# Optimization experiments

Measured on AMD Instinct MI355X. Metric: run time of the kernel, lower is better.

Reference implementation:

```python
import jax, jax.numpy as jnp
import numpy as np

B, S, D, H = 2, 2048, 2048, 16
DK = D // H


def setup_inputs() -> dict:
    key = jax.random.key(0)
    k1, k2, k3 = jax.random.split(key, 3)
    x = jax.random.normal(k1, (B, S, D), dtype=jnp.float32)
    # trunc-normal in the original; plain normal with matching std is fine for a numeric baseline
    std_qkv = 2.0 / (DK + D)  # note: original passes variance as std to trunc_normal_
    W_qkv = jax.random.normal(k2, (3 * D, D), dtype=jnp.float32) * std_qkv
    W_o = jax.random.normal(k3, (D, D), dtype=jnp.float32) * (1.0 / D)
    return {"x": x, "W_qkv": W_qkv, "W_o": W_o}


def reference(x, W_qkv, W_o):
    b, s, d = x.shape
    # fused QKV projection: y = x @ W_qkv^T
    qkv = jnp.einsum('bsd,ed->bse', x, W_qkv)  # [b, s, 3d]
    q, k, v = jnp.split(qkv, 3, axis=-1)
    # [b, s, d] -> [b, h, s, dk]
    def to_heads(t):
        return t.reshape(b, s, H, DK).transpose(0, 2, 1, 3)
    q, k, v = to_heads(q), to_heads(k), to_heads(v)
    scores = jnp.einsum('bhqd,bhkd->bhqk', q, k) / np.sqrt(DK).astype(np.float32)
    causal = jnp.tril(jnp.ones((s, s), dtype=bool))
    scores = jnp.where(causal, scores, -jnp.inf)
    att = jax.nn.softmax(scores, axis=-1)
    out = jnp.einsum('bhqk,bhkd->bhqd', att, v)  # [b, h, s, dk]
    out = out.transpose(0, 2, 1, 3).reshape(b, s, d)
    return jnp.einsum('bsd,od->bso', out, W_o)
```

## Files before the change

kernel.cpp:

```cpp
#include <hip/hip_runtime.h>

typedef _Float16 f16;
typedef _Float16 f16x4 __attribute__((ext_vector_type(4)));
typedef _Float16 f16x8 __attribute__((ext_vector_type(8)));
typedef float    f32x4 __attribute__((ext_vector_type(4)));

#define MFMA_F16(a,b,c) __builtin_amdgcn_mfma_f32_16x16x32_f16((a),(b),(c),0,0,0)

static constexpr int B_  = 2;
static constexpr int S_  = 2048;
static constexpr int D_  = 2048;
static constexpr int H_  = 16;
static constexpr int DK_ = 128;
static constexpr int K_  = 2048;

__device__ __forceinline__ void gload_lds16(const void* g, void* l) {
  __builtin_amdgcn_global_load_lds(
      (const __attribute__((address_space(1))) void*)g,
      (__attribute__((address_space(3))) void*)l, 16, 0, 0);
}

__global__ __launch_bounds__(256) void cast_f16_kernel(const float* __restrict__ in,
                                                       f16* __restrict__ out, int n4) {
  int i = blockIdx.x * 256 + threadIdx.x;
  int stride = gridDim.x * 256;
  for (int j = i; j < n4; j += stride) {
    float4 v = reinterpret_cast<const float4*>(in)[j];
    f16x4 o = {(f16)v.x, (f16)v.y, (f16)v.z, (f16)v.w};
    reinterpret_cast<f16x4*>(out)[j] = o;
  }
}

__device__ __forceinline__ void gemm_core(const f16* __restrict__ A, const f16* __restrict__ Bw,
                                          int brow, int bcol, f16* As, f16* Bs,
                                          f32x4 (&acc)[4][4]) {
  const int tid = threadIdx.x;
  const int w = tid >> 6, l = tid & 63;
  const int lg = l >> 4, lr = l & 15;
  const int wr = w >> 1, wc = w & 1;
#pragma unroll
  for (int mi = 0; mi < 4; ++mi)
#pragma unroll
    for (int ni = 0; ni < 4; ++ni) acc[mi][ni] = (f32x4){0.f, 0.f, 0.f, 0.f};

  const int rA = brow * 128 + (l >> 2);
  const int rB = bcol * 128 + (l >> 2);
  const int ck = (l & 3) * 8;

  for (int kt = 0; kt < K_ / 32; ++kt) {
    __syncthreads();
#pragma unroll
    for (int i = 0; i < 2; ++i) {
      const int c = w + i * 4;
      gload_lds16(A  + (size_t)(rA + c * 16) * K_ + kt * 32 + ck, As + c * 512);
      gload_lds16(Bw + (size_t)(rB + c * 16) * K_ + kt * 32 + ck, Bs + c * 512);
    }
    __syncthreads();
    f16x8 af[4], bf[4];
#pragma unroll
    for (int mi = 0; mi < 4; ++mi)
      af[mi] = *(const f16x8*)(As + (wr * 64 + mi * 16 + lr) * 32 + lg * 8);
#pragma unroll
    for (int ni = 0; ni < 4; ++ni)
      bf[ni] = *(const f16x8*)(Bs + (wc * 64 + ni * 16 + lr) * 32 + lg * 8);
#pragma unroll
    for (int mi = 0; mi < 4; ++mi)
#pragma unroll
      for (int ni = 0; ni < 4; ++ni)
        acc[mi][ni] = MFMA_F16(af[mi], bf[ni], acc[mi][ni]);
  }
}

__global__ __launch_bounds__(256) void gemm_qkv_kernel(const f16* __restrict__ xb,
                                                       const f16* __restrict__ wqkv,
                                                       f16* __restrict__ Q,
                                                       f16* __restrict__ Kk,
                                                       f16* __restrict__ V) {
  __shared__ __align__(16) f16 As[4096];
  __shared__ __align__(16) f16 Bs[4096];
  const int bid = blockIdx.x;
  const int swz = (bid & 7) * (1536 / 8) + (bid >> 3);
  const int brow = swz / 48, bcol = swz % 48;

  f32x4 acc[4][4];
  gemm_core(xb, wqkv, brow, bcol, As, Bs, acc);

  const int tid = threadIdx.x;
  const int w = tid >> 6, l = tid & 63;
  const int lg = l >> 4, lr = l & 15;
  const int wr = w >> 1, wc = w & 1;

  const int which = bcol / 16;
  const int h = bcol % 16;
  f16* outp = (which == 0) ? Q : ((which == 1) ? Kk : V);
  const float scale = (which == 0) ? 0.08838834764831845f : 1.0f;

#pragma unroll
  for (int mi = 0; mi < 4; ++mi) {
    const int mbase = brow * 128 + wr * 64 + mi * 16 + lg * 4;
#pragma unroll
    for (int ni = 0; ni < 4; ++ni) {
      const int dk = wc * 64 + ni * 16 + lr;
#pragma unroll
      for (int r = 0; r < 4; ++r) {
        const int mm = mbase + r;
        const int b = mm >> 11, s = mm & 2047;
        outp[(((size_t)b * H_ + h) * S_ + s) * DK_ + dk] = (f16)(acc[mi][ni][r] * scale);
      }
    }
  }
}

__global__ __launch_bounds__(256) void gemm_out_kernel(const f16* __restrict__ ab,
                                                       const f16* __restrict__ wo,
                                                       float* __restrict__ out) {
  __shared__ __align__(16) f16 As[4096];
  __shared__ __align__(16) f16 Bs[4096];
  const int bid = blockIdx.x;
  const int swz = (bid & 7) * (512 / 8) + (bid >> 3);
  const int brow = swz / 16, bcol = swz % 16;

  f32x4 acc[4][4];
  gemm_core(ab, wo, brow, bcol, As, Bs, acc);

  const int tid = threadIdx.x;
  const int w = tid >> 6, l = tid & 63;
  const int lg = l >> 4, lr = l & 15;
  const int wr = w >> 1, wc = w & 1;

#pragma unroll
  for (int mi = 0; mi < 4; ++mi) {
    const int mbase = brow * 128 + wr * 64 + mi * 16 + lg * 4;
#pragma unroll
    for (int ni = 0; ni < 4; ++ni) {
      const int n = bcol * 128 + wc * 64 + ni * 16 + lr;
#pragma unroll
      for (int r = 0; r < 4; ++r)
        out[(size_t)(mbase + r) * D_ + n] = acc[mi][ni][r];
    }
  }
}

__global__ __launch_bounds__(256) void transpose_v_kernel(const f16* __restrict__ V,
                                                          f16* __restrict__ Vt) {
  const int bid = blockIdx.x;
  const int dt = bid & 1;
  const int st = (bid >> 1) & 31;
  const int bh = bid >> 6;
  __shared__ __align__(16) f16 t[64][72];
  const int tid = threadIdx.x;
#pragma unroll
  for (int i = 0; i < 2; ++i) {
    const int chunk = i * 256 + tid;
    const int row = chunk >> 3, c8 = chunk & 7;
    f16x8 v = *(const f16x8*)(V + ((size_t)bh * S_ + st * 64 + row) * DK_ + dt * 64 + c8 * 8);
    *(f16x8*)&t[row][c8 * 8] = v;
  }
  __syncthreads();
#pragma unroll
  for (int i = 0; i < 2; ++i) {
    const int chunk = i * 256 + tid;
    const int row = chunk >> 3, c8 = chunk & 7;
    f16x8 v;
#pragma unroll
    for (int jj = 0; jj < 8; ++jj) v[jj] = t[c8 * 8 + jj][row];
    *(f16x8*)(Vt + ((size_t)bh * DK_ + dt * 64 + row) * S_ + st * 64 + c8 * 8) = v;
  }
}

__global__ __launch_bounds__(256) void attn_kernel(const f16* __restrict__ Q,
                                                   const f16* __restrict__ Kg,
                                                   const f16* __restrict__ Vt,
                                                   f16* __restrict__ O) {
  __shared__ __align__(16) unsigned char Ks[64 * 256];
  __shared__ __align__(16) unsigned char Vs[128 * 128];
  __shared__ __align__(16) unsigned char Ps[4][16 * 128];

  const int bid = blockIdx.x;
  const int pr = bid & 15;
  const int h  = (bid >> 4) & 15;
  const int b  = bid >> 8;
  const int bh = b * H_ + h;
  const int tid = threadIdx.x;
  const int w = tid >> 6, l = tid & 63;
  const int lg = l >> 4, lr = l & 15;

  for (int half = 0; half < 2; ++half) {
    const int qt = half ? (31 - pr) : pr;

    const f16* Qg = Q + ((size_t)bh * S_ + qt * 64 + w * 16) * DK_;
    f16x8 qf[4];
#pragma unroll
    for (int kd = 0; kd < 4; ++kd)
      qf[kd] = *(const f16x8*)(Qg + (size_t)lr * DK_ + kd * 32 + lg * 8);

    f32x4 o[8];
#pragma unroll
    for (int n = 0; n < 8; ++n) o[n] = (f32x4){0.f, 0.f, 0.f, 0.f};
    float mrun[4] = {-1e30f, -1e30f, -1e30f, -1e30f};
    float lrun[4] = {0.f, 0.f, 0.f, 0.f};

    const int ntiles = qt + 1;
    for (int kt = 0; kt < ntiles; ++kt) {
      __syncthreads();
      const f16* Kt = Kg + ((size_t)bh * S_ + kt * 64) * DK_;
#pragma unroll
      for (int i = 0; i < 4; ++i) {
        const int chunk = i * 256 + tid;
        const int row = chunk >> 4, c8 = chunk & 15;
        uint4 v = *(const uint4*)(Kt + (size_t)row * DK_ + c8 * 8);
        *(uint4*)(Ks + row * 256 + ((c8 * 16) ^ ((row & 7) << 4))) = v;
      }
      const f16* Vtt = Vt + (size_t)bh * DK_ * S_ + kt * 64;
#pragma unroll
      for (int i = 0; i < 4; ++i) {
        const int chunk = i * 256 + tid;
        const int row = chunk >> 3, c8 = chunk & 7;
        uint4 v = *(const uint4*)(Vtt + (size_t)row * S_ + c8 * 8);
        *(uint4*)(Vs + row * 128 + ((c8 * 16) ^ ((row & 7) << 4))) = v;
      }
      __syncthreads();

      f32x4 s[4];
#pragma unroll
      for (int j = 0; j < 4; ++j) s[j] = (f32x4){0.f, 0.f, 0.f, 0.f};
#pragma unroll
      for (int j = 0; j < 4; ++j) {
        const int row = j * 16 + lr;
#pragma unroll
        for (int kd = 0; kd < 4; ++kd) {
          f16x8 kf = *(const f16x8*)(Ks + row * 256 + ((kd * 64 + lg * 16) ^ ((row & 7) << 4)));
          s[j] = MFMA_F16(qf[kd], kf, s[j]);
        }
      }
      if (kt == qt) {
#pragma unroll
        for (int j = 0; j < 4; ++j) {
          const int col = j * 16 + lr;
#pragma unroll
          for (int r = 0; r < 4; ++r) {
            const int qrow = w * 16 + lg * 4 + r;
            if (col > qrow) s[j][r] = -1e30f;
          }
        }
      }
      float scl[4];
#pragma unroll
      for (int r = 0; r < 4; ++r) {
        float m0 = fmaxf(fmaxf(s[0][r], s[1][r]), fmaxf(s[2][r], s[3][r]));
#pragma unroll
        for (int msk = 1; msk < 16; msk <<= 1) m0 = fmaxf(m0, __shfl_xor(m0, msk, 64));
        const float nm = fmaxf(mrun[r], m0);
        scl[r] = __expf(mrun[r] - nm);
        mrun[r] = nm;
      }
      float rs[4] = {0.f, 0.f, 0.f, 0.f};
#pragma unroll
      for (int j = 0; j < 4; ++j) {
#pragma unroll
        for (int r = 0; r < 4; ++r) {
          const float p = __expf(fmaxf(s[j][r] - mrun[r], -80.f));
          rs[r] += p;
          const int row = lg * 4 + r;
          const int cb = (j * 16 + lr) * 2;
          *(f16*)(Ps[w] + row * 128 + (cb ^ ((row & 7) << 4))) = (f16)p;
        }
      }
#pragma unroll
      for (int r = 0; r < 4; ++r) {
        float t = rs[r];
#pragma unroll
        for (int msk = 1; msk < 16; msk <<= 1) t += __shfl_xor(t, msk, 64);
        lrun[r] = lrun[r] * scl[r] + t;
      }
#pragma unroll
      for (int n = 0; n < 8; ++n)
#pragma unroll
        for (int r = 0; r < 4; ++r) o[n][r] *= scl[r];

      asm volatile("s_waitcnt lgkmcnt(0)" ::: "memory");

#pragma unroll
      for (int ks = 0; ks < 2; ++ks) {
        f16x8 pf = *(const f16x8*)(Ps[w] + lr * 128 + ((ks * 64 + lg * 16) ^ ((lr & 7) << 4)));
#pragma unroll
        for (int n = 0; n < 8; ++n) {
          const int row = n * 16 + lr;
          f16x8 vf = *(const f16x8*)(Vs + row * 128 + ((ks * 64 + lg * 16) ^ ((row & 7) << 4)));
          o[n] = MFMA_F16(pf, vf, o[n]);
        }
      }
    }

#pragma unroll
    for (int r = 0; r < 4; ++r) {
      const float inv = 1.0f / lrun[r];
      const int srow = qt * 64 + w * 16 + lg * 4 + r;
      f16* op = O + ((size_t)b * S_ + srow) * D_ + h * DK_;
#pragma unroll
      for (int n = 0; n < 8; ++n) op[n * 16 + lr] = (f16)(o[n][r] * inv);
    }
  }
}

extern "C" void kernel_launch(void* const* d_in, const int* in_sizes, int n_in,
                              void* d_out, int out_size, void* d_ws, size_t ws_size,
                              hipStream_t stream) {
  const float* x    = (const float*)d_in[0];
  const float* wqkv = (const float*)d_in[1];
  const float* wo   = (const float*)d_in[2];
  float* out = (float*)d_out;
  char* ws = (char*)d_ws;

  f16* xb     = (f16*)(ws + 0);
  f16* wqkvb  = (f16*)(ws + 16777216);
  f16* wob    = (f16*)(ws + 41943040);
  f16* Qb     = (f16*)(ws + 50331648);
  f16* Kb     = (f16*)(ws + 67108864);
  f16* Vb     = (f16*)(ws + 83886080);
  f16* Vtb    = (f16*)(ws + 16777216);
  f16* attn_o = (f16*)(ws + 0);

  cast_f16_kernel<<<2048, 256, 0, stream>>>(x, xb, 8388608 / 4);
  cast_f16_kernel<<<2048, 256, 0, stream>>>(wqkv, wqkvb, 12582912 / 4);
  cast_f16_kernel<<<1024, 256, 0, stream>>>(wo, wob, 4194304 / 4);

  gemm_qkv_kernel<<<1536, 256, 0, stream>>>(xb, wqkvb, Qb, Kb, Vb);
  transpose_v_kernel<<<2048, 256, 0, stream>>>(Vb, Vtb);
  attn_kernel<<<512, 256, 0, stream>>>(Qb, Kb, Vtb, attn_o);
  gemm_out_kernel<<<512, 256, 0, stream>>>(attn_o, wob, out);
}
```

Before: 305.1 us.

## Pipeline GEMM loads with triple-buffered LDS ring, fuse V transpose, raise MFMA priority

Replaces the single-buffered GEMM core with a three-slot LDS ring that prefetches two k-tiles ahead, using vmcnt waits and raw barriers, plus an XOR-swizzled LDS layout. The QKV GEMM now writes V directly in transposed layout, which removes the separate transpose kernel and its round trip through memory. MFMA blocks in the GEMM and attention kernels are wrapped in setprio. The 48KB of LDS per block and the launch bound of three blocks per CU cap occupancy, and the transposed V stores are narrow strided writes.

```diff
diff --git a/kernel.cpp b/kernel.cpp
--- a/kernel.cpp
+++ b/kernel.cpp
@@ -13,6 +13,7 @@
 static constexpr int H_  = 16;
 static constexpr int DK_ = 128;
 static constexpr int K_  = 2048;
+static constexpr int NKT = 64;
 
 __device__ __forceinline__ void gload_lds16(const void* g, void* l) {
   __builtin_amdgcn_global_load_lds(
@@ -31,59 +32,97 @@
   }
 }
 
-__device__ __forceinline__ void gemm_core(const f16* __restrict__ A, const f16* __restrict__ Bw,
-                                          int brow, int bcol, f16* As, f16* Bs,
-                                          f32x4 (&acc)[4][4]) {
+
+__device__ __forceinline__ void ring_stage3(const f16* gA, const f16* gB, int t,
+                                            char* slot, int w) {
+  gload_lds16(gA + (size_t)(w * 16) * K_ + t * 32,        slot + w * 1024);
+  gload_lds16(gA + (size_t)((w + 4) * 16) * K_ + t * 32,  slot + (w + 4) * 1024);
+  gload_lds16(gB + (size_t)(w * 16) * K_ + t * 32,        slot + 8192 + w * 1024);
+  gload_lds16(gB + (size_t)((w + 4) * 16) * K_ + t * 32,  slot + 8192 + (w + 4) * 1024);
+}
+
+__device__ __forceinline__ void ring_step3(const char* slot, int wr, int wc, int lro,
+                                           f32x4 (&acc)[4][4]) {
+  f16x8 af[4], bf[4];
+#pragma unroll
+  for (int mi = 0; mi < 4; ++mi)
+    af[mi] = *(const f16x8*)(slot + (wr * 4 + mi) * 1024 + lro);
+#pragma unroll
+  for (int ni = 0; ni < 4; ++ni)
+    bf[ni] = *(const f16x8*)(slot + 8192 + (wc * 4 + ni) * 1024 + lro);
+  __builtin_amdgcn_s_setprio(1);
+#pragma unroll
+  for (int mi = 0; mi < 4; ++mi)
+#pragma unroll
+    for (int ni = 0; ni < 4; ++ni)
+      acc[mi][ni] = MFMA_F16(af[mi], bf[ni], acc[mi][ni]);
+  __builtin_amdgcn_s_setprio(0);
+}
+
+#define SYNC3(N)                                              \
+  asm volatile("s_waitcnt vmcnt(" #N ")" ::: "memory");       \
+  __builtin_amdgcn_s_barrier();                               \
+  asm volatile("" ::: "memory");
+
+#define STEP3(CS, TT, SS)                                     \
+  ring_stage3(gA, gB, (TT), (SS), w);                         \
+  ring_step3((CS), wr, wc, lro, acc);                         \
+  SYNC3(4)
+
+__device__ __forceinline__ void gemm_core3(const f16* __restrict__ A,
+                                           const f16* __restrict__ Bw,
+                                           int brow, int bcol, char* lds,
+                                           f32x4 (&acc)[4][4]) {
   const int tid = threadIdx.x;
   const int w = tid >> 6, l = tid & 63;
   const int lg = l >> 4, lr = l & 15;
   const int wr = w >> 1, wc = w & 1;
+  const int lro = (lr * 4 + (lg ^ ((lr >> 1) & 3))) * 16;
+
 #pragma unroll
   for (int mi = 0; mi < 4; ++mi)
 #pragma unroll
     for (int ni = 0; ni < 4; ++ni) acc[mi][ni] = (f32x4){0.f, 0.f, 0.f, 0.f};
 
-  const int rA = brow * 128 + (l >> 2);
-  const int rB = bcol * 128 + (l >> 2);
-  const int ck = (l & 3) * 8;
-
-  for (int kt = 0; kt < K_ / 32; ++kt) {
-    __syncthreads();
-#pragma unroll
-    for (int i = 0; i < 2; ++i) {
-      const int c = w + i * 4;
-      gload_lds16(A  + (size_t)(rA + c * 16) * K_ + kt * 32 + ck, As + c * 512);
-      gload_lds16(Bw + (size_t)(rB + c * 16) * K_ + kt * 32 + ck, Bs + c * 512);
-    }
-    __syncthreads();
-    f16x8 af[4], bf[4];
-#pragma unroll
-    for (int mi = 0; mi < 4; ++mi)
-      af[mi] = *(const f16x8*)(As + (wr * 64 + mi * 16 + lr) * 32 + lg * 8);
-#pragma unroll
-    for (int ni = 0; ni < 4; ++ni)
-      bf[ni] = *(const f16x8*)(Bs + (wc * 64 + ni * 16 + lr) * 32 + lg * 8);
-#pragma unroll
-    for (int mi = 0; mi < 4; ++mi)
-#pragma unroll
-      for (int ni = 0; ni < 4; ++ni)
-        acc[mi][ni] = MFMA_F16(af[mi], bf[ni], acc[mi][ni]);
-  }
-}
-
-__global__ __launch_bounds__(256) void gemm_qkv_kernel(const f16* __restrict__ xb,
-                                                       const f16* __restrict__ wqkv,
-                                                       f16* __restrict__ Q,
-                                                       f16* __restrict__ Kk,
-                                                       f16* __restrict__ V) {
-  __shared__ __align__(16) f16 As[4096];
-  __shared__ __align__(16) f16 Bs[4096];
+  const int kgsrc = (l & 3) ^ ((l >> 3) & 3);
+  const f16* gA = A  + (size_t)(brow * 128 + (l >> 2)) * K_ + kgsrc * 8;
+  const f16* gB = Bw + (size_t)(bcol * 128 + (l >> 2)) * K_ + kgsrc * 8;
+
+  char* s0 = lds;
+  char* s1 = lds + 16384;
+  char* s2 = lds + 32768;
+
+  ring_stage3(gA, gB, 0, s0, w);
+  ring_stage3(gA, gB, 1, s1, w);
+  SYNC3(4)
+
+  for (int tb = 0; tb < 20; ++tb) {
+    const int t = 3 * tb;
+    STEP3(s0, t + 2, s2)
+    STEP3(s1, t + 3, s0)
+    STEP3(s2, t + 4, s1)
+  }
+  STEP3(s0, 62, s2)
+  STEP3(s1, 63, s0)
+  ring_step3(s2, wr, wc, lro, acc);
+  asm volatile("s_waitcnt vmcnt(0)" ::: "memory");
+  __builtin_amdgcn_s_barrier();
+  asm volatile("" ::: "memory");
+  ring_step3(s0, wr, wc, lro, acc);
+}
+
+__global__ __launch_bounds__(256, 3) void gemm_qkv_kernel(const f16* __restrict__ xb,
+                                                          const f16* __restrict__ wqkv,
+                                                          f16* __restrict__ Q,
+                                                          f16* __restrict__ Kk,
+                                                          f16* __restrict__ Vt) {
+  __shared__ __align__(16) char lds[49152];
   const int bid = blockIdx.x;
-  const int swz = (bid & 7) * (1536 / 8) + (bid >> 3);
+  const int swz = (bid & 7) * 192 + (bid >> 3);
   const int brow = swz / 48, bcol = swz % 48;
 
   f32x4 acc[4][4];
-  gemm_core(xb, wqkv, brow, bcol, As, Bs, acc);
+  gemm_core3(xb, wqkv, brow, bcol, lds, acc);
 
   const int tid = threadIdx.x;
   const int w = tid >> 6, l = tid & 63;
@@ -92,36 +131,50 @@
 
   const int which = bcol / 16;
   const int h = bcol % 16;
-  f16* outp = (which == 0) ? Q : ((which == 1) ? Kk : V);
-  const float scale = (which == 0) ? 0.08838834764831845f : 1.0f;
-
-#pragma unroll
-  for (int mi = 0; mi < 4; ++mi) {
-    const int mbase = brow * 128 + wr * 64 + mi * 16 + lg * 4;
-#pragma unroll
-    for (int ni = 0; ni < 4; ++ni) {
-      const int dk = wc * 64 + ni * 16 + lr;
-#pragma unroll
-      for (int r = 0; r < 4; ++r) {
-        const int mm = mbase + r;
-        const int b = mm >> 11, s = mm & 2047;
-        outp[(((size_t)b * H_ + h) * S_ + s) * DK_ + dk] = (f16)(acc[mi][ni][r] * scale);
-      }
-    }
-  }
-}
-
-__global__ __launch_bounds__(256) void gemm_out_kernel(const f16* __restrict__ ab,
-                                                       const f16* __restrict__ wo,
-                                                       float* __restrict__ out) {
-  __shared__ __align__(16) f16 As[4096];
-  __shared__ __align__(16) f16 Bs[4096];
+
+  if (which == 2) {
+#pragma unroll
+    for (int mi = 0; mi < 4; ++mi) {
+      const int mbase = brow * 128 + wr * 64 + mi * 16 + lg * 4;
+      const int b = mbase >> 11, s = mbase & 2047;
+#pragma unroll
+      for (int ni = 0; ni < 4; ++ni) {
+        const int dk = wc * 64 + ni * 16 + lr;
+        f16x4 v = {(f16)acc[mi][ni][0], (f16)acc[mi][ni][1],
+                   (f16)acc[mi][ni][2], (f16)acc[mi][ni][3]};
+        *(f16x4*)(Vt + ((size_t)(b * H_ + h) * DK_ + dk) * S_ + s) = v;
+      }
+    }
+  } else {
+    f16* outp = (which == 0) ? Q : Kk;
+    const float scale = (which == 0) ? 0.08838834764831845f : 1.0f;
+#pragma unroll
+    for (int mi = 0; mi < 4; ++mi) {
+      const int mbase = brow * 128 + wr * 64 + mi * 16 + lg * 4;
+#pragma unroll
+      for (int ni = 0; ni < 4; ++ni) {
+        const int dk = wc * 64 + ni * 16 + lr;
+#pragma unroll
+        for (int r = 0; r < 4; ++r) {
+          const int mm = mbase + r;
+          const int b = mm >> 11, s = mm & 2047;
+          outp[(((size_t)b * H_ + h) * S_ + s) * DK_ + dk] = (f16)(acc[mi][ni][r] * scale);
+        }
+      }
+    }
+  }
+}
+
+__global__ __launch_bounds__(256, 3) void gemm_out_kernel(const f16* __restrict__ ab,
+                                                          const f16* __restrict__ wo,
+                                                          float* __restrict__ out) {
+  __shared__ __align__(16) char lds[49152];
   const int bid = blockIdx.x;
-  const int swz = (bid & 7) * (512 / 8) + (bid >> 3);
+  const int swz = (bid & 7) * 64 + (bid >> 3);
   const int brow = swz / 16, bcol = swz % 16;
 
   f32x4 acc[4][4];
-  gemm_core(ab, wo, brow, bcol, As, Bs, acc);
+  gemm_core3(ab, wo, brow, bcol, lds, acc);
 
   const int tid = threadIdx.x;
   const int w = tid >> 6, l = tid & 63;
@@ -138,33 +191,6 @@
       for (int r = 0; r < 4; ++r)
         out[(size_t)(mbase + r) * D_ + n] = acc[mi][ni][r];
     }
-  }
-}
-
-__global__ __launch_bounds__(256) void transpose_v_kernel(const f16* __restrict__ V,
-                                                          f16* __restrict__ Vt) {
-  const int bid = blockIdx.x;
-  const int dt = bid & 1;
-  const int st = (bid >> 1) & 31;
-  const int bh = bid >> 6;
-  __shared__ __align__(16) f16 t[64][72];
-  const int tid = threadIdx.x;
-#pragma unroll
-  for (int i = 0; i < 2; ++i) {
-    const int chunk = i * 256 + tid;
-    const int row = chunk >> 3, c8 = chunk & 7;
-    f16x8 v = *(const f16x8*)(V + ((size_t)bh * S_ + st * 64 + row) * DK_ + dt * 64 + c8 * 8);
-    *(f16x8*)&t[row][c8 * 8] = v;
-  }
-  __syncthreads();
-#pragma unroll
-  for (int i = 0; i < 2; ++i) {
-    const int chunk = i * 256 + tid;
-    const int row = chunk >> 3, c8 = chunk & 7;
-    f16x8 v;
-#pragma unroll
-    for (int jj = 0; jj < 8; ++jj) v[jj] = t[c8 * 8 + jj][row];
-    *(f16x8*)(Vt + ((size_t)bh * DK_ + dt * 64 + row) * S_ + st * 64 + c8 * 8) = v;
   }
 }
 
@@ -224,6 +250,7 @@
       f32x4 s[4];
 #pragma unroll
       for (int j = 0; j < 4; ++j) s[j] = (f32x4){0.f, 0.f, 0.f, 0.f};
+      __builtin_amdgcn_s_setprio(1);
 #pragma unroll
       for (int j = 0; j < 4; ++j) {
         const int row = j * 16 + lr;
@@ -233,6 +260,7 @@
           s[j] = MFMA_F16(qf[kd], kf, s[j]);
         }
       }
+      __builtin_amdgcn_s_setprio(0);
       if (kt == qt) {
 #pragma unroll
         for (int j = 0; j < 4; ++j) {
@@ -280,6 +308,7 @@
 
       asm volatile("s_waitcnt lgkmcnt(0)" ::: "memory");
 
+      __builtin_amdgcn_s_setprio(1);
 #pragma unroll
       for (int ks = 0; ks < 2; ++ks) {
         f16x8 pf = *(const f16x8*)(Ps[w] + lr * 128 + ((ks * 64 + lg * 16) ^ ((lr & 7) << 4)));
@@ -290,6 +319,7 @@
           o[n] = MFMA_F16(pf, vf, o[n]);
         }
       }
+      __builtin_amdgcn_s_setprio(0);
     }
 
 #pragma unroll
@@ -317,16 +347,14 @@
   f16* wob    = (f16*)(ws + 41943040);
   f16* Qb     = (f16*)(ws + 50331648);
   f16* Kb     = (f16*)(ws + 67108864);
-  f16* Vb     = (f16*)(ws + 83886080);
-  f16* Vtb    = (f16*)(ws + 16777216);
+  f16* Vtb    = (f16*)(ws + 83886080);
   f16* attn_o = (f16*)(ws + 0);
 
   cast_f16_kernel<<<2048, 256, 0, stream>>>(x, xb, 8388608 / 4);
   cast_f16_kernel<<<2048, 256, 0, stream>>>(wqkv, wqkvb, 12582912 / 4);
   cast_f16_kernel<<<1024, 256, 0, stream>>>(wo, wob, 4194304 / 4);
 
-  gemm_qkv_kernel<<<1536, 256, 0, stream>>>(xb, wqkvb, Qb, Kb, Vb);
-  transpose_v_kernel<<<2048, 256, 0, stream>>>(Vb, Vtb);
+  gemm_qkv_kernel<<<1536, 256, 0, stream>>>(xb, wqkvb, Qb, Kb, Vtb);
   attn_kernel<<<512, 256, 0, stream>>>(Qb, Kb, Vtb, attn_o);
   gemm_out_kernel<<<512, 256, 0, stream>>>(attn_o, wob, out);
 }
```

After: 299.8 us. Within noise of the previous version (-1.8%).
